# Performance work log

Measured on AMD Instinct MI355X. Metric: run time of the kernel, lower is better.

The kernel has to match this reference:

```python
import jax, jax.numpy as jnp
import numpy as np

N, E = 100000, 1600000
D_IN, D_HID, D_OUT = 128, 64, 64
NEG_SLOPE = 0.2


def setup_inputs() -> dict:
    key = jax.random.key(0)
    ks = jax.random.split(key, 12)
    x = jax.random.normal(ks[0], (N, D_IN), dtype=jnp.float32)
    edge_index = jax.random.randint(ks[1], (2, E), 0, N, dtype=jnp.int64)
    edge_attr = jax.random.normal(ks[2], (E, 8), dtype=jnp.float32)
    s1 = 1.0 / np.sqrt(D_IN)
    s2 = 1.0 / np.sqrt(D_HID)
    return {
        "x": x,
        "edge_index": edge_index,
        "edge_attr": edge_attr,
        "W1": jax.random.normal(ks[3], (D_IN, D_HID), dtype=jnp.float32) * s1,
        "att_src1": jax.random.normal(ks[4], (D_HID,), dtype=jnp.float32) * s2,
        "att_dst1": jax.random.normal(ks[5], (D_HID,), dtype=jnp.float32) * s2,
        "b1": jnp.zeros((D_HID,), dtype=jnp.float32),
        "W2": jax.random.normal(ks[6], (D_HID, D_OUT), dtype=jnp.float32) * s2,
        "att_src2": jax.random.normal(ks[7], (D_OUT,), dtype=jnp.float32) * (1.0 / np.sqrt(D_OUT)),
        "att_dst2": jax.random.normal(ks[8], (D_OUT,), dtype=jnp.float32) * (1.0 / np.sqrt(D_OUT)),
        "b2": jnp.zeros((D_OUT,), dtype=jnp.float32),
    }


def gat_conv(x, src, dst, W, att_src, att_dst, b, n_nodes):
    # h = W x  (single head)
    h = x @ W                                   # [N, F]
    a_src = h @ att_src                         # [N]
    a_dst = h @ att_dst                         # [N]
    e = jax.nn.leaky_relu(a_src[src] + a_dst[dst], NEG_SLOPE)  # [E]
    # softmax over incoming edges per target node (numerically stable)
    e_max = jax.ops.segment_max(e, dst, num_segments=n_nodes)
    w = jnp.exp(e - e_max[dst])
    denom = jax.ops.segment_sum(w, dst, num_segments=n_nodes)
    alpha = w / (denom[dst] + 1e-16)            # [E]
    out = jax.ops.segment_sum(h[src] * alpha[:, None], dst, num_segments=n_nodes)
    return out + b


def reference(x, edge_index, edge_attr, W1, att_src1, att_dst1, b1, W2, att_src2, att_dst2, b2):
    n_nodes = x.shape[0]
    # PyG GATConv default: add self-loops; edge_attr unused (edge_dim=None)
    loops = jnp.arange(n_nodes, dtype=edge_index.dtype)
    src = jnp.concatenate([edge_index[0], loops])
    dst = jnp.concatenate([edge_index[1], loops])
    h = gat_conv(x, src, dst, W1, att_src1, att_dst1, b1, n_nodes)
    h = jax.nn.relu(h)
    h = gat_conv(h, src, dst, W2, att_src2, att_dst2, b2, n_nodes)
    # global_mean_pool with batch=None -> mean over all nodes, shape [1, D_OUT]
    return jnp.mean(h, axis=0, keepdims=True)
```

## Files before the change

### kernel.cpp

```cpp
#include <hip/hip_runtime.h>
#include <hip/hip_bf16.h>
#include <cstdint>

#define NEG_SLOPE 0.2f
#define SCAN_ELEMS 1024
#define BUCKET_SHIFT 9
#define CHUNK 8192

typedef __attribute__((ext_vector_type(4))) int            i32x4;
typedef __attribute__((ext_vector_type(4))) float          f32x4;
typedef __attribute__((ext_vector_type(8))) unsigned short u16x8;
typedef __attribute__((ext_vector_type(4))) unsigned short u16x4;

__device__ inline unsigned short f2bf(float f) {
    unsigned xi = __float_as_uint(f);
    unsigned r = xi + 0x7fffu + ((xi >> 16) & 1u);
    return (unsigned short)(r >> 16);
}
__device__ inline float bflo(unsigned g) { return __uint_as_float(g << 16); }
__device__ inline float bfhi(unsigned g) { return __uint_as_float(g & 0xffff0000u); }

__device__ inline int get_ei(const int* ei, int is64, long idx) {
    return is64 ? ei[2 * idx] : ei[(int)idx];
}

__device__ inline int detect_is64(const int* __restrict__ ei, int tid) {
    __shared__ int dred[4];
    int v = 0;
    for (int i = tid; i < 2048; i += 256) v |= ei[2 * i + 1];
#pragma unroll
    for (int off = 32; off; off >>= 1) v |= __shfl_xor(v, off);
    if ((tid & 63) == 0) dred[tid >> 6] = v;
    __syncthreads();
    int r = dred[0] | dred[1] | dred[2] | dred[3];
    __syncthreads();
    return (r == 0) ? 1 : 0;
}

__global__ __launch_bounds__(256) void p1_hist(const int* __restrict__ ei,
                                               int* __restrict__ HH,
                                               int E, int n, int nblk) {
    __shared__ int cnt[256];
    int tid = threadIdx.x;
    int is64 = detect_is64(ei, tid);
    int nbuk = (n + (1 << BUCKET_SHIFT) - 1) >> BUCKET_SHIFT;
    for (int b = tid; b < nbuk; b += 256) cnt[b] = 0;
    __syncthreads();
    int total = E + n;
    int beg = blockIdx.x * CHUNK;
    int end = beg + CHUNK; if (end > total) end = total;
    for (int i = beg + tid; i < end; i += 256) {
        int d = (i < E) ? get_ei(ei, is64, (long)E + i) : (i - E);
        atomicAdd(&cnt[d >> BUCKET_SHIFT], 1);
    }
    __syncthreads();
    for (int b = tid; b < nbuk; b += 256) HH[b * nblk + blockIdx.x] = cnt[b];
}

__global__ __launch_bounds__(256) void scan1_kernel(const int* __restrict__ src,
                                                    int* __restrict__ bsums, int n) {
    int t = threadIdx.x;
    int i0 = blockIdx.x * SCAN_ELEMS + 4 * t;
    int4 v = make_int4(0, 0, 0, 0);
    if (i0 + 3 < n) v = *(const int4*)(src + i0);
    else {
        if (i0 + 0 < n) v.x = src[i0 + 0];
        if (i0 + 1 < n) v.y = src[i0 + 1];
        if (i0 + 2 < n) v.z = src[i0 + 2];
        if (i0 + 3 < n) v.w = src[i0 + 3];
    }
    int s = v.x + v.y + v.z + v.w;
#pragma unroll
    for (int off = 32; off; off >>= 1) s += __shfl_down(s, off);
    __shared__ int ws[4];
    if ((t & 63) == 0) ws[t >> 6] = s;
    __syncthreads();
    if (t == 0) bsums[blockIdx.x] = ws[0] + ws[1] + ws[2] + ws[3];
}

__global__ __launch_bounds__(256) void scan3g_kernel(const int* __restrict__ src,
                                                     const int* __restrict__ bsums,
                                                     int* __restrict__ out, int n, int nb) {
    int b = blockIdx.x;
    int t = threadIdx.x;
    __shared__ int sb[256];
    int bv = (t < nb) ? bsums[t] : 0;
    sb[t] = bv;
    __syncthreads();
    for (int off = 1; off < 256; off <<= 1) {
        int u = (t >= off) ? sb[t - off] : 0;
        __syncthreads();
        sb[t] += u;
        __syncthreads();
    }
    int blockbase = (b == 0) ? 0 : sb[b - 1];

    int i0 = b * SCAN_ELEMS + 4 * t;
    int4 v = make_int4(0, 0, 0, 0);
    if (i0 + 3 < n) v = *(const int4*)(src + i0);
    else {
        if (i0 + 0 < n) v.x = src[i0 + 0];
        if (i0 + 1 < n) v.y = src[i0 + 1];
        if (i0 + 2 < n) v.z = src[i0 + 2];
        if (i0 + 3 < n) v.w = src[i0 + 3];
    }
    int s0 = v.x, s1 = s0 + v.y, s2 = s1 + v.z, s3 = s2 + v.w;
    __shared__ int sh[256];
    sh[t] = s3;
    __syncthreads();
    for (int off = 1; off < 256; off <<= 1) {
        int u = (t >= off) ? sh[t - off] : 0;
        __syncthreads();
        sh[t] += u;
        __syncthreads();
    }
    int base = blockbase + sh[t] - s3;
    if (i0 + 0 < n) out[i0 + 0] = base;
    if (i0 + 1 < n) out[i0 + 1] = base + s0;
    if (i0 + 2 < n) out[i0 + 2] = base + s1;
    if (i0 + 3 < n) out[i0 + 3] = base + s2;
}

__global__ __launch_bounds__(256) void p3_scatter(const int* __restrict__ ei,
                                                  const int* __restrict__ scanHH,
                                                  int* __restrict__ sorted,
                                                  int E, int n, int nblk) {
    __shared__ int base[256];
    __shared__ int cur[256];
    int tid = threadIdx.x;
    int is64 = detect_is64(ei, tid);
    int nbuk = (n + (1 << BUCKET_SHIFT) - 1) >> BUCKET_SHIFT;
    for (int b = tid; b < nbuk; b += 256) {
        base[b] = scanHH[b * nblk + blockIdx.x];
        cur[b] = 0;
    }
    __syncthreads();
    int total = E + n;
    int beg = blockIdx.x * CHUNK;
    int end = beg + CHUNK; if (end > total) end = total;
    for (int i = beg + tid; i < end; i += 256) {
        int s, d;
        if (i < E) {
            s = get_ei(ei, is64, i);
            d = get_ei(ei, is64, (long)E + i);
        } else {
            s = d = i - E;
        }
        int b = d >> BUCKET_SHIFT;
        int p = base[b] + atomicAdd(&cur[b], 1);
        sorted[p] = (s << BUCKET_SHIFT) | (d & ((1 << BUCKET_SHIFT) - 1));
    }
}

__global__ __launch_bounds__(256) void p4_finalize(const int* __restrict__ scanHH,
                                                   const int* __restrict__ sorted,
                                                   int* __restrict__ ptr,
                                                   int* __restrict__ csr_src,
                                                   int n, int nblk, int T) {
    int b = blockIdx.x;
    int nbuk = gridDim.x;
    int tid = threadIdx.x;
    int node0 = b << BUCKET_SHIFT;
    int nn = n - node0; if (nn > (1 << BUCKET_SHIFT)) nn = 1 << BUCKET_SHIFT;
    int beg = scanHH[b * nblk];
    int end = (b + 1 < nbuk) ? scanHH[(b + 1) * nblk] : T;

    __shared__ int cnt[512];
    __shared__ int pair[256];
    __shared__ int exc[512];
    cnt[tid] = 0; cnt[tid + 256] = 0;
    __syncthreads();
    for (int j = beg + tid; j < end; j += 256) {
        int v = sorted[j];
        atomicAdd(&cnt[v & ((1 << BUCKET_SHIFT) - 1)], 1);
    }
    __syncthreads();
    int psum = cnt[2 * tid] + cnt[2 * tid + 1];
    pair[tid] = psum;
    __syncthreads();
    for (int off = 1; off < 256; off <<= 1) {
        int u = (tid >= off) ? pair[tid - off] : 0;
        __syncthreads();
        pair[tid] += u;
        __syncthreads();
    }
    int pexc = pair[tid] - psum;
    exc[2 * tid] = pexc;
    exc[2 * tid + 1] = pexc + cnt[2 * tid];
    __syncthreads();
    for (int i = tid; i < nn; i += 256) ptr[node0 + i] = beg + exc[i];
    if (node0 + nn == n && tid == 0) ptr[n] = T;
    cnt[tid] = exc[tid]; cnt[tid + 256] = exc[tid + 256];
    __syncthreads();
    for (int j = beg + tid; j < end; j += 256) {
        int v = sorted[j];
        int p = beg + atomicAdd(&cnt[v & ((1 << BUCKET_SHIFT) - 1)], 1);
        csr_src[p] = ((unsigned)v) >> BUCKET_SHIFT;
    }
}

__global__ __launch_bounds__(256) void pack_w(const float* __restrict__ W1,
                                              const float* __restrict__ W2,
                                              unsigned short* __restrict__ wp1,
                                              unsigned short* __restrict__ wp2) {
    int t = blockIdx.x * 256 + threadIdx.x;
    if (t >= 24 * 64) return;
    int f = t >> 6, l = t & 63;
    int lm = l & 15, lg = l >> 4;
    const float* W = (f < 16) ? W1 : W2;
    unsigned short* wp = (f < 16) ? wp1 : wp2;
    int idx = (f < 16) ? f : (f - 16);
    int kt = idx >> 2, ct = idx & 3;
    union { u16x8 v; unsigned short u[8]; } o;
#pragma unroll
    for (int e = 0; e < 8; ++e)
        o.u[e] = f2bf(W[(size_t)(32 * kt + 8 * lg + e) * 64 + 16 * ct + lm]);
    *(u16x8*)(wp + ((size_t)idx * 64 + l) * 8) = o.v;
}

#define MFMA_BF16(acc, a, b) \
    asm("s_nop 1\n\tv_mfma_f32_16x16x32_bf16 %0, %1, %2, %0" \
        : "+v"(acc) : "v"(a), "v"(b))

template <int KT, bool XBF>
__global__ __launch_bounds__(256) void proj_mfma(const void* __restrict__ xin,
                                                 const unsigned short* __restrict__ Wp,
                                                 const float* __restrict__ att_s,
                                                 const float* __restrict__ att_d,
                                                 unsigned short* __restrict__ h2,
                                                 float* __restrict__ asrc,
                                                 float* __restrict__ adst, int n) {
    constexpr int K = 32 * KT;
    __shared__ alignas(16) unsigned short lb[4][16 * 72];
    int tid = threadIdx.x;
    int wid = tid >> 6, l = tid & 63;
    int lm = l & 15, lg = l >> 4;

    int node0 = blockIdx.x * 64 + wid * 16;
    if (node0 >= n) return;

    float as_c[4], ad_c[4];
#pragma unroll
    for (int ct = 0; ct < 4; ++ct) {
        as_c[ct] = att_s[16 * ct + lm];
        ad_c[ct] = att_d[16 * ct + lm];
    }

    f32x4 acc[4] = {};

    int arow = node0 + lm;
    bool rowok = arow < n;

#pragma unroll
    for (int kt = 0; kt < KT; ++kt) {
        i32x4 af = {0, 0, 0, 0};
        if (XBF) {
            const unsigned short* xb = (const unsigned short*)xin
                                       + (size_t)arow * K + 32 * kt + 8 * lg;
            if (rowok) af = *(const i32x4*)xb;
        } else {
            const float* xp = (const float*)xin + (size_t)arow * K + 8 * lg + 32 * kt;
            float4 v0 = make_float4(0.f, 0.f, 0.f, 0.f);
            float4 v1 = v0;
            if (rowok) {
                v0 = *(const float4*)(xp);
                v1 = *(const float4*)(xp + 4);
            }
            af[0] = (int)((unsigned)f2bf(v0.x) | ((unsigned)f2bf(v0.y) << 16));
            af[1] = (int)((unsigned)f2bf(v0.z) | ((unsigned)f2bf(v0.w) << 16));
            af[2] = (int)((unsigned)f2bf(v1.x) | ((unsigned)f2bf(v1.y) << 16));
            af[3] = (int)((unsigned)f2bf(v1.z) | ((unsigned)f2bf(v1.w) << 16));
        }
#pragma unroll
        for (int ct = 0; ct < 4; ++ct) {
            i32x4 bf = *(const i32x4*)(Wp + (((kt * 4 + ct) * 64) + l) * 8);
            MFMA_BF16(acc[ct], af, bf);
        }
    }
    asm volatile("s_nop 7\n\ts_nop 7"
                 : "+v"(acc[0]), "+v"(acc[1]), "+v"(acc[2]), "+v"(acc[3]));

    float ps[4], pd[4];
#pragma unroll
    for (int r = 0; r < 4; ++r) {
        float s = 0.f, d = 0.f;
#pragma unroll
        for (int ct = 0; ct < 4; ++ct) {
            s = fmaf(acc[ct][r], as_c[ct], s);
            d = fmaf(acc[ct][r], ad_c[ct], d);
        }
        ps[r] = s; pd[r] = d;
    }
#pragma unroll
    for (int off = 1; off < 16; off <<= 1) {
#pragma unroll
        for (int r = 0; r < 4; ++r) {
            ps[r] += __shfl_xor(ps[r], off);
            pd[r] += __shfl_xor(pd[r], off);
        }
    }
    if (lm == 0) {
#pragma unroll
        for (int r = 0; r < 4; ++r) {
            int node = node0 + 4 * lg + r;
            if (node < n) { asrc[node] = ps[r]; adst[node] = pd[r]; }
        }
    }

    unsigned short* wb = lb[wid];
#pragma unroll
    for (int ct = 0; ct < 4; ++ct)
#pragma unroll
        for (int r = 0; r < 4; ++r)
            wb[(4 * lg + r) * 72 + 16 * ct + lm] = f2bf(acc[ct][r]);
    asm volatile("s_waitcnt lgkmcnt(0)" ::: "memory");
    int ch = l & 7;
#pragma unroll
    for (int p = 0; p < 2; ++p) {
        int rr = (l >> 3) + 8 * p;
        u16x8 ov = *(const u16x8*)(wb + rr * 72 + 8 * ch);
        int onode = node0 + rr;
        if (onode < n)
            *(u16x8*)(h2 + (size_t)onode * 64 + 8 * ch) = ov;
    }
}

template <bool FMEAN>
__global__ __launch_bounds__(256) void agg_kernel(const int* __restrict__ ptr,
                                                  const int* __restrict__ srcs,
                                                  const unsigned short* __restrict__ h2,
                                                  const float* __restrict__ asrc,
                                                  const float* __restrict__ adst,
                                                  const float* __restrict__ bias,
                                                  unsigned short* __restrict__ outbf,
                                                  float* __restrict__ partials,
                                                  int n, int do_relu) {
    __shared__ int2  sm[4][64];
    __shared__ float red[256];
    int tid = threadIdx.x;
    int lane = tid & 63, wid = tid >> 6;
    int slot = lane >> 4, f = lane & 15;
    const char* h2b = (const char*)h2;
    unsigned fo = (unsigned)f << 3;
    float4 bv = *(const float4*)(bias + 4 * f);
    float ms0 = 0.f, ms1 = 0.f, ms2 = 0.f, ms3 = 0.f;

    int gwave = (blockIdx.x * blockDim.x + tid) >> 6;
    int nwaves = (gridDim.x * blockDim.x) >> 6;
    for (int node = gwave; node < n; node += nwaves) {
        int beg = ptr[node], end = ptr[node + 1];
        float ad = adst[node];
        float a0 = 0.f, a1 = 0.f, a2 = 0.f, a3 = 0.f, wsum = 0.f;
        for (int b = beg; b < end; b += 64) {
            int blen = end - b; if (blen > 64) blen = 64;
            int sv = 0; float wv = 0.f;
            if (lane < blen) {
                sv = srcs[b + lane];
                float e = asrc[sv] + ad;
                e = (e > 0.f) ? e : NEG_SLOPE * e;
                wv = __expf(e);
            }
            wsum += wv;
            sm[wid][lane] = make_int2(sv, __float_as_int(wv));
            int ni = (blen + 7) >> 3;
            for (int j = 0; j < ni; ++j) {
#pragma unroll
                for (int u = 0; u < 2; ++u) {
                    int e0 = 8 * j + 4 * u + slot;
                    int2 swp = sm[wid][e0];
                    float w = __int_as_float(swp.y);
                    uint2 g = *(const uint2*)(h2b + (((unsigned)swp.x << 7) + fo));
                    a0 = fmaf(w, bflo(g.x), a0);
                    a1 = fmaf(w, bfhi(g.x), a1);
                    a2 = fmaf(w, bflo(g.y), a2);
                    a3 = fmaf(w, bfhi(g.y), a3);
                }
            }
        }
        a0 += __shfl_xor(a0, 16); a0 += __shfl_xor(a0, 32);
        a1 += __shfl_xor(a1, 16); a1 += __shfl_xor(a1, 32);
        a2 += __shfl_xor(a2, 16); a2 += __shfl_xor(a2, 32);
        a3 += __shfl_xor(a3, 16); a3 += __shfl_xor(a3, 32);
#pragma unroll
        for (int off = 32; off; off >>= 1) wsum += __shfl_xor(wsum, off);
        float inv = 1.f / (wsum + 1e-16f);
        float o0 = a0 * inv + bv.x;
        float o1 = a1 * inv + bv.y;
        float o2 = a2 * inv + bv.z;
        float o3 = a3 * inv + bv.w;
        if (!FMEAN) {
            if (do_relu) {
                o0 = fmaxf(o0, 0.f); o1 = fmaxf(o1, 0.f);
                o2 = fmaxf(o2, 0.f); o3 = fmaxf(o3, 0.f);
            }
            if (slot == 0) {
                u16x4 ov;
                ov[0] = f2bf(o0); ov[1] = f2bf(o1);
                ov[2] = f2bf(o2); ov[3] = f2bf(o3);
                *(u16x4*)(outbf + (size_t)node * 64 + 4 * f) = ov;
            }
        } else {
            if (slot == 0) { ms0 += o0; ms1 += o1; ms2 += o2; ms3 += o3; }
        }
    }
    if (FMEAN) {
        if (slot == 0)
            *(float4*)(red + wid * 64 + 4 * f) = make_float4(ms0, ms1, ms2, ms3);
        __syncthreads();
        if (tid < 64) {
            float t = red[tid] + red[64 + tid] + red[128 + tid] + red[192 + tid];
            partials[(size_t)blockIdx.x * 64 + tid] = t;
        }
    }
}

__global__ __launch_bounds__(256) void reduce_mean(const float* __restrict__ partials,
                                                   float* __restrict__ out,
                                                   int nb, float inv_n) {
    __shared__ float red[256];
    int f = threadIdx.x & 63;
    int w = threadIdx.x >> 6;
    int idx = blockIdx.x * 4 + w;
    int stride = gridDim.x * 4;
    float s = 0.f;
    for (int r = idx; r < nb; r += stride) s += partials[(size_t)r * 64 + f];
    red[threadIdx.x] = s;
    __syncthreads();
    if (w == 0) {
        float t = red[f] + red[64 + f] + red[128 + f] + red[192 + f];
        atomicAdd(&out[f], t * inv_n);
    }
}

extern "C" void kernel_launch(void* const* d_in, const int* in_sizes, int n_in,
                              void* d_out, int out_size, void* d_ws, size_t ws_size,
                              hipStream_t stream) {
    const float* x   = (const float*)d_in[0];
    const int*   ei  = (const int*)d_in[1];
    const float* W1  = (const float*)d_in[3];
    const float* as1 = (const float*)d_in[4];
    const float* ad1 = (const float*)d_in[5];
    const float* b1  = (const float*)d_in[6];
    const float* W2  = (const float*)d_in[7];
    const float* as2 = (const float*)d_in[8];
    const float* ad2 = (const float*)d_in[9];
    const float* b2  = (const float*)d_in[10];
    float* out = (float*)d_out;

    const int N = in_sizes[0] / 128;
    const int E = in_sizes[1] / 2;
    const int T = E + N;

    const int NBUK = (N + (1 << BUCKET_SHIFT) - 1) >> BUCKET_SHIFT;
    const int NBLK = (T + CHUNK - 1) / CHUNK;
    const int NHH  = NBUK * NBLK;
    const int NBS  = (NHH + SCAN_ELEMS - 1) / SCAN_ELEMS;
    const int AGRID = (N + 3) / 4;

    size_t off = 0;
    char* base = (char*)d_ws;
    auto alloc = [&](size_t bytes) -> void* {
        void* p = base + off;
        off += (bytes + 255) & ~(size_t)255;
        return p;
    };
    int*   ptr     = (int*)alloc(((size_t)N + 1) * 4);
    int*   bsums   = (int*)alloc(256 * 4);
    int*   HH      = (int*)alloc((size_t)NHH * 4);
    int*   scanHH  = (int*)alloc((size_t)NHH * 4);
    int*   csr_src = (int*)alloc((size_t)T * 4);
    float* asrc    = (float*)alloc((size_t)N * 4);
    float* adst    = (float*)alloc((size_t)N * 4);
    unsigned short* h2 = (unsigned short*)alloc((size_t)N * 64 * 2);
    unsigned short* bufB = (unsigned short*)alloc((size_t)N * 64 * 4);
    unsigned short* wp1 = (unsigned short*)alloc(16 * 64 * 8 * 2);
    unsigned short* wp2 = (unsigned short*)alloc(8 * 64 * 8 * 2);
    int*   sorted  = (int*)bufB;
    float* partials = (float*)bufB;
    (void)ws_size;

    pack_w<<<6, 256, 0, stream>>>(W1, W2, wp1, wp2);

    p1_hist<<<NBLK, 256, 0, stream>>>(ei, HH, E, N, NBLK);
    scan1_kernel<<<NBS, 256, 0, stream>>>(HH, bsums, NHH);
    scan3g_kernel<<<NBS, 256, 0, stream>>>(HH, bsums, scanHH, NHH, NBS);
    p3_scatter<<<NBLK, 256, 0, stream>>>(ei, scanHH, sorted, E, N, NBLK);
    p4_finalize<<<NBUK, 256, 0, stream>>>(scanHH, sorted, ptr, csr_src, N, NBLK, T);

    const int PGRID = (N + 63) / 64;

    proj_mfma<4, false><<<PGRID, 256, 0, stream>>>(x, wp1, as1, ad1, h2, asrc, adst, N);
    agg_kernel<false><<<AGRID, 256, 0, stream>>>(ptr, csr_src, h2, asrc, adst,
                                                 b1, bufB, nullptr, N, 1);

    proj_mfma<2, true><<<PGRID, 256, 0, stream>>>(bufB, wp2, as2, ad2, h2, asrc, adst, N);
    agg_kernel<true><<<AGRID, 256, 0, stream>>>(ptr, csr_src, h2, asrc, adst,
                                                b2, nullptr, partials, N, 0);
    hipMemsetAsync(out, 0, 64 * 4, stream);
    reduce_mean<<<64, 256, 0, stream>>>(partials, out, AGRID, 1.f / (float)N);
}
```

Before: 346.0 us.

## Precompute per-edge attention weights in a separate edge-parallel kernel before aggregation

Adds an edge_w kernel that computes exp(leaky_relu(asrc[s]+adst[d])) for every edge into a packed (src, weight) array. To support this, the CSR build now stores destination alongside source. The aggregation kernel reads these precomputed pairs directly, drops the LDS staging step, and processes four edges per slot for more memory-level parallelism. This takes the dependent asrc gather and exp off the aggregation critical path. In exchange it adds extra global traffic: writing and re-reading 8-byte pairs per edge, a wider CSR array, and two extra launches.

```diff
diff --git a/kernel.cpp b/kernel.cpp
--- a/kernel.cpp
+++ b/kernel.cpp
@@ -155,7 +155,7 @@
 __global__ __launch_bounds__(256) void p4_finalize(const int* __restrict__ scanHH,
                                                    const int* __restrict__ sorted,
                                                    int* __restrict__ ptr,
-                                                   int* __restrict__ csr_src,
+                                                   int2* __restrict__ csr_sd,
                                                    int n, int nblk, int T) {
     int b = blockIdx.x;
     int nbuk = gridDim.x;
@@ -194,8 +194,9 @@
     __syncthreads();
     for (int j = beg + tid; j < end; j += 256) {
         int v = sorted[j];
-        int p = beg + atomicAdd(&cnt[v & ((1 << BUCKET_SHIFT) - 1)], 1);
-        csr_src[p] = ((unsigned)v) >> BUCKET_SHIFT;
+        int d9 = v & ((1 << BUCKET_SHIFT) - 1);
+        int p = beg + atomicAdd(&cnt[d9], 1);
+        csr_sd[p] = make_int2((int)(((unsigned)v) >> BUCKET_SHIFT), node0 + d9);
     }
 }
 
@@ -325,17 +326,42 @@
     }
 }
 
+__global__ __launch_bounds__(256) void edge_w(const int2* __restrict__ sd,
+                                              const float* __restrict__ asrc,
+                                              const float* __restrict__ adst,
+                                              int2* __restrict__ sw, int T) {
+    int i = 4 * (blockIdx.x * 256 + threadIdx.x);
+    int stride = 4 * gridDim.x * 256;
+    for (; i + 3 < T; i += stride) {
+        int2 e[4];
+#pragma unroll
+        for (int u = 0; u < 4; ++u) e[u] = sd[i + u];
+        float s[4], d[4];
+#pragma unroll
+        for (int u = 0; u < 4; ++u) { s[u] = asrc[e[u].x]; d[u] = adst[e[u].y]; }
+#pragma unroll
+        for (int u = 0; u < 4; ++u) {
+            float v = s[u] + d[u];
+            v = (v > 0.f) ? v : NEG_SLOPE * v;
+            sw[i + u] = make_int2(e[u].x, __float_as_int(__expf(v)));
+        }
+    }
+    for (int k = i; k < T && k < i + 4; ++k) {
+        int2 ev = sd[k];
+        float v = asrc[ev.x] + adst[ev.y];
+        v = (v > 0.f) ? v : NEG_SLOPE * v;
+        sw[k] = make_int2(ev.x, __float_as_int(__expf(v)));
+    }
+}
+
 template <bool FMEAN>
 __global__ __launch_bounds__(256) void agg_kernel(const int* __restrict__ ptr,
-                                                  const int* __restrict__ srcs,
+                                                  const int2* __restrict__ sw,
                                                   const unsigned short* __restrict__ h2,
-                                                  const float* __restrict__ asrc,
-                                                  const float* __restrict__ adst,
                                                   const float* __restrict__ bias,
                                                   unsigned short* __restrict__ outbf,
                                                   float* __restrict__ partials,
                                                   int n, int do_relu) {
-    __shared__ int2  sm[4][64];
     __shared__ float red[256];
     int tid = threadIdx.x;
     int lane = tid & 63, wid = tid >> 6;
@@ -349,31 +375,32 @@
     int nwaves = (gridDim.x * blockDim.x) >> 6;
     for (int node = gwave; node < n; node += nwaves) {
         int beg = ptr[node], end = ptr[node + 1];
-        float ad = adst[node];
         float a0 = 0.f, a1 = 0.f, a2 = 0.f, a3 = 0.f, wsum = 0.f;
         for (int b = beg; b < end; b += 64) {
             int blen = end - b; if (blen > 64) blen = 64;
-            int sv = 0; float wv = 0.f;
-            if (lane < blen) {
-                sv = srcs[b + lane];
-                float e = asrc[sv] + ad;
-                e = (e > 0.f) ? e : NEG_SLOPE * e;
-                wv = __expf(e);
-            }
-            wsum += wv;
-            sm[wid][lane] = make_int2(sv, __float_as_int(wv));
-            int ni = (blen + 7) >> 3;
+            int ni = (blen + 15) >> 4;
             for (int j = 0; j < ni; ++j) {
-#pragma unroll
-                for (int u = 0; u < 2; ++u) {
-                    int e0 = 8 * j + 4 * u + slot;
-                    int2 swp = sm[wid][e0];
-                    float w = __int_as_float(swp.y);
-                    uint2 g = *(const uint2*)(h2b + (((unsigned)swp.x << 7) + fo));
-                    a0 = fmaf(w, bflo(g.x), a0);
-                    a1 = fmaf(w, bfhi(g.x), a1);
-                    a2 = fmaf(w, bflo(g.y), a2);
-                    a3 = fmaf(w, bfhi(g.y), a3);
+                int e0 = b + 16 * j + slot;
+                int2 swv[4];
+#pragma unroll
+                for (int u = 0; u < 4; ++u) {
+                    int e = e0 + 4 * u;
+                    int ec = (e < end) ? e : end - 1;
+                    swv[u] = sw[ec];
+                }
+                uint2 g[4]; float w[4];
+#pragma unroll
+                for (int u = 0; u < 4; ++u) {
+                    w[u] = (e0 + 4 * u < end) ? __int_as_float(swv[u].y) : 0.f;
+                    g[u] = *(const uint2*)(h2b + (((unsigned)swv[u].x << 7) + fo));
+                }
+#pragma unroll
+                for (int u = 0; u < 4; ++u) {
+                    wsum += w[u];
+                    a0 = fmaf(w[u], bflo(g[u].x), a0);
+                    a1 = fmaf(w[u], bfhi(g[u].x), a1);
+                    a2 = fmaf(w[u], bflo(g[u].y), a2);
+                    a3 = fmaf(w[u], bfhi(g[u].y), a3);
                 }
             }
         }
@@ -381,8 +408,7 @@
         a1 += __shfl_xor(a1, 16); a1 += __shfl_xor(a1, 32);
         a2 += __shfl_xor(a2, 16); a2 += __shfl_xor(a2, 32);
         a3 += __shfl_xor(a3, 16); a3 += __shfl_xor(a3, 32);
-#pragma unroll
-        for (int off = 32; off; off >>= 1) wsum += __shfl_xor(wsum, off);
+        wsum += __shfl_xor(wsum, 16); wsum += __shfl_xor(wsum, 32);
         float inv = 1.f / (wsum + 1e-16f);
         float o0 = a0 * inv + bv.x;
         float o1 = a1 * inv + bv.y;
@@ -468,7 +494,8 @@
     int*   bsums   = (int*)alloc(256 * 4);
     int*   HH      = (int*)alloc((size_t)NHH * 4);
     int*   scanHH  = (int*)alloc((size_t)NHH * 4);
-    int*   csr_src = (int*)alloc((size_t)T * 4);
+    int2*  csr_sd  = (int2*)alloc((size_t)T * 8);
+    int2*  sw      = (int2*)alloc((size_t)T * 8);
     float* asrc    = (float*)alloc((size_t)N * 4);
     float* adst    = (float*)alloc((size_t)N * 4);
     unsigned short* h2 = (unsigned short*)alloc((size_t)N * 64 * 2);
@@ -485,17 +512,18 @@
     scan1_kernel<<<NBS, 256, 0, stream>>>(HH, bsums, NHH);
     scan3g_kernel<<<NBS, 256, 0, stream>>>(HH, bsums, scanHH, NHH, NBS);
     p3_scatter<<<NBLK, 256, 0, stream>>>(ei, scanHH, sorted, E, N, NBLK);
-    p4_finalize<<<NBUK, 256, 0, stream>>>(scanHH, sorted, ptr, csr_src, N, NBLK, T);
+    p4_finalize<<<NBUK, 256, 0, stream>>>(scanHH, sorted, ptr, csr_sd, N, NBLK, T);
 
     const int PGRID = (N + 63) / 64;
+    const int EWGRID = (T + 1023) / 1024;
 
     proj_mfma<4, false><<<PGRID, 256, 0, stream>>>(x, wp1, as1, ad1, h2, asrc, adst, N);
-    agg_kernel<false><<<AGRID, 256, 0, stream>>>(ptr, csr_src, h2, asrc, adst,
-                                                 b1, bufB, nullptr, N, 1);
+    edge_w<<<EWGRID, 256, 0, stream>>>(csr_sd, asrc, adst, sw, T);
+    agg_kernel<false><<<AGRID, 256, 0, stream>>>(ptr, sw, h2, b1, bufB, nullptr, N, 1);
 
     proj_mfma<2, true><<<PGRID, 256, 0, stream>>>(bufB, wp2, as2, ad2, h2, asrc, adst, N);
-    agg_kernel<true><<<AGRID, 256, 0, stream>>>(ptr, csr_src, h2, asrc, adst,
-                                                b2, nullptr, partials, N, 0);
+    edge_w<<<EWGRID, 256, 0, stream>>>(csr_sd, asrc, adst, sw, T);
+    agg_kernel<true><<<AGRID, 256, 0, stream>>>(ptr, sw, h2, b2, nullptr, partials, N, 0);
     hipMemsetAsync(out, 0, 64 * 4, stream);
     reduce_mean<<<64, 256, 0, stream>>>(partials, out, AGRID, 1.f / (float)N);
 }
```

Result: slower. 368.9 us (+6.6%).
